# Kernel optimization log

Hardware: AMD Instinct MI355X
Metric: run time of the kernel (lower is better)

Reference implementation:

```python
import jax, jax.numpy as jnp
import numpy as np

N_NODES = 100000
N_HEDGES = 200000
E = 1200000
N_GRAPHS = 512
H = 64            # h_dim
HE = 35           # hedge_fea_dim (CHGConv default)
HOUT = 128        # hout_dim
L = 3             # n_layers
EPS = 1e-5


def _segment_mean(vals, seg, num):
    s = jax.ops.segment_sum(vals, seg, num_segments=num)
    cnt = jax.ops.segment_sum(jnp.ones((vals.shape[0], 1), vals.dtype), seg, num_segments=num)
    return s / jnp.maximum(cnt, 1.0)


def _bn(v, g, b):
    # BatchNorm1d in training mode: batch mean / biased variance
    m = jnp.mean(v, axis=0)
    var = jnp.var(v, axis=0)
    return g * (v - m) * jax.lax.rsqrt(var + EPS) + b


def _chg_conv(x, node_idx, hedge_idx, hattr,
              Wf1, bf1, Wc1, bc1, Wf2, bf2, Wc2, bc2,
              gf, btf, gc, btc, go, bto):
    # gather node feats into hedges, mean-aggregate per hyperedge
    agg = _segment_mean(x[node_idx], hedge_idx, N_HEDGES)          # [NH, H]
    msg = jnp.concatenate([agg, hattr], axis=1)                    # [NH, H+HE]
    z_f = _bn(msg @ Wf1 + bf1, gf, btf)
    z_c = _bn(msg @ Wc1 + bc1, gc, btc)
    hedge_feats = jax.nn.sigmoid(z_f) * jax.nn.softplus(z_c)       # [NH, HE]
    z = jnp.concatenate([x[node_idx], hedge_feats[hedge_idx]], axis=-1)  # [E, H+HE]
    out = jax.nn.sigmoid(z @ Wf2 + bf2) * jax.nn.softplus(z @ Wc2 + bc2)  # [E, H]
    out = _segment_mean(out, node_idx, N_NODES)                    # [N, H]
    out = _bn(out, go, bto)
    return jax.nn.softplus(out + x)


def setup_inputs() -> dict:
    key = jax.random.key(0)
    ks = jax.random.split(key, 32)
    x = jax.random.normal(ks[0], (N_NODES, 92), dtype=jnp.float32)
    node_idx = jax.random.randint(ks[1], (E,), 0, N_NODES)
    hedge_idx = jax.random.randint(ks[2], (E,), 0, N_HEDGES)
    hyperedge_index = jnp.stack([node_idx, hedge_idx], axis=0)     # [2, E]
    hedge_attr = jax.random.normal(ks[3], (N_HEDGES, HE), dtype=jnp.float32)
    batch = jnp.sort(jax.random.randint(ks[4], (N_NODES,), 0, N_GRAPHS))

    s = 0.05
    d = H + HE
    inp = {
        'x': x, 'hyperedge_index': hyperedge_index, 'hedge_attr': hedge_attr, 'batch': batch,
        'We': jax.random.normal(ks[5], (92, H)) * s, 'be': jnp.zeros((H,)),
        'Wf1': jax.random.normal(ks[6], (L, d, HE)) * s, 'bf1': jnp.zeros((L, HE)),
        'Wc1': jax.random.normal(ks[7], (L, d, HE)) * s, 'bc1': jnp.zeros((L, HE)),
        'Wf2': jax.random.normal(ks[8], (L, d, H)) * s, 'bf2': jnp.zeros((L, H)),
        'Wc2': jax.random.normal(ks[9], (L, d, H)) * s, 'bc2': jnp.zeros((L, H)),
        'bn_f_g': jnp.ones((L, HE)), 'bn_f_b': jnp.zeros((L, HE)),
        'bn_c_g': jnp.ones((L, HE)), 'bn_c_b': jnp.zeros((L, HE)),
        'bn_o_g': jnp.ones((L, H)), 'bn_o_b': jnp.zeros((L, H)),
        'Wl2': jax.random.normal(ks[10], (H, HOUT)) * s, 'bl2': jnp.zeros((HOUT,)),
        'Wo': jax.random.normal(ks[11], (HOUT, 1)) * s, 'bo': jnp.zeros((1,)),
    }
    return inp


def reference(x, hyperedge_index, hedge_attr, batch, We, be,
              Wf1, bf1, Wc1, bc1, Wf2, bf2, Wc2, bc2,
              bn_f_g, bn_f_b, bn_c_g, bn_c_b, bn_o_g, bn_o_b,
              Wl2, bl2, Wo, bo):
    node_idx = hyperedge_index[0]
    hedge_idx = hyperedge_index[1]
    h = x @ We + be                                                # embed 92 -> H
    for i in range(L):                                             # only mconvs are used in forward
        h = _chg_conv(h, node_idx, hedge_idx, hedge_attr,
                      Wf1[i], bf1[i], Wc1[i], bc1[i], Wf2[i], bf2[i], Wc2[i], bc2[i],
                      bn_f_g[i], bn_f_b[i], bn_c_g[i], bn_c_b[i], bn_o_g[i], bn_o_b[i])
        h = jax.nn.relu(h)
    g = _segment_mean(h, batch, N_GRAPHS)                          # [G, H]
    g = jax.nn.softplus(g @ Wl2 + bl2)                             # [G, HOUT]
    return g @ Wo + bo                                             # [G, 1]
```

## Files before the change

### kernel.cpp

```cpp
#include <hip/hip_runtime.h>
#include <cstddef>

#define N_NODES_  100000
#define N_HEDGES_ 200000
#define E_        1200000
#define G_        512
#define H_        64
#define HE_       35
#define D_        99
#define HOUT_     128
#define L_        3
#define NBN5_     196
#define NBH5_     391
#define CHUNK_    4096

typedef unsigned int u32;
typedef _Float16 f2_t __attribute__((ext_vector_type(2)));

__device__ __forceinline__ float sigm_(float x){
  return __builtin_amdgcn_rcpf(1.f + __expf(-x));
}
__device__ __forceinline__ float sp_(float x){
  return fmaxf(x, 0.f) + __logf(1.f + __expf(-fabsf(x)));
}
__device__ __forceinline__ float gate_(float F, float C){ return sigm_(F)*sp_(C); }

__device__ __forceinline__ u32 pk_(float a, float b){
  return __builtin_bit_cast(u32, __builtin_amdgcn_cvt_pkrtz(a, b));
}
__device__ __forceinline__ u32 pkadd_(u32 a, u32 b){
  f2_t s = __builtin_bit_cast(f2_t, a) + __builtin_bit_cast(f2_t, b);
  return __builtin_bit_cast(u32, s);
}
__device__ __forceinline__ float dot2_(u32 a, u32 b, float c){
#if __has_builtin(__builtin_amdgcn_fdot2)
  return __builtin_amdgcn_fdot2(__builtin_bit_cast(f2_t, a),
                                __builtin_bit_cast(f2_t, b), c, false);
#else
  f2_t x = __builtin_bit_cast(f2_t, a), y = __builtin_bit_cast(f2_t, b);
  return c + (float)x[0]*(float)y[0] + (float)x[1]*(float)y[1];
#endif
}
__device__ __forceinline__ float lo_(u32 a){ return (float)__builtin_bit_cast(f2_t, a)[0]; }
__device__ __forceinline__ float hi_(u32 a){ return (float)__builtin_bit_cast(f2_t, a)[1]; }

__global__ void k_gcnt(const int* __restrict__ batch, int* __restrict__ gcnt){
  int n = blockIdx.x*256 + threadIdx.x;
  if (n < N_NODES_) atomicAdd(&gcnt[batch[n]], 1);
}
__global__ void k_gscan(const int* __restrict__ gcnt, int* __restrict__ goff){
  __shared__ int tmp[512];
  int t = threadIdx.x;
  int v = gcnt[t];
  tmp[t] = v; __syncthreads();
  for (int d = 1; d < 512; d <<= 1){
    int x = (t >= d) ? tmp[t-d] : 0; __syncthreads();
    tmp[t] += x; __syncthreads();
  }
  goff[t] = tmp[t] - v;
  if (t == 511) goff[512] = tmp[511];
}

__global__ void k_bhist(const int* __restrict__ ni, const int* __restrict__ hi,
                        int* __restrict__ totN, int* __restrict__ totH){
  __shared__ int hN[NBN5_], hH[NBH5_];
  for (int i = threadIdx.x; i < NBN5_; i += 256) hN[i] = 0;
  for (int i = threadIdx.x; i < NBH5_; i += 256) hH[i] = 0;
  __syncthreads();
  int stride = gridDim.x*256;
  for (int e = blockIdx.x*256 + threadIdx.x; e < E_; e += stride){
    atomicAdd(&hN[ni[e] >> 9], 1);
    atomicAdd(&hH[hi[e] >> 9], 1);
  }
  __syncthreads();
  for (int i = threadIdx.x; i < NBN5_; i += 256) if (hN[i]) atomicAdd(&totN[i], hN[i]);
  for (int i = threadIdx.x; i < NBH5_; i += 256) if (hH[i]) atomicAdd(&totH[i], hH[i]);
}

__global__ void k_bscan(const int* __restrict__ totN, const int* __restrict__ totH,
                        int* __restrict__ bbaseN, int* __restrict__ bbaseH,
                        int* __restrict__ gcurN, int* __restrict__ gcurH){
  __shared__ int tmp[512];
  int t = threadIdx.x;
  int v = (t < NBN5_) ? totN[t] : 0;
  tmp[t] = v; __syncthreads();
  for (int d = 1; d < 512; d <<= 1){
    int x = (t >= d) ? tmp[t-d] : 0; __syncthreads();
    tmp[t] += x; __syncthreads();
  }
  if (t < NBN5_){ int b = tmp[t] - v; bbaseN[t] = b; gcurN[t] = b; }
  __syncthreads();
  int w = (t < NBH5_) ? totH[t] : 0;
  tmp[t] = w; __syncthreads();
  for (int d = 1; d < 512; d <<= 1){
    int x = (t >= d) ? tmp[t-d] : 0; __syncthreads();
    tmp[t] += x; __syncthreads();
  }
  if (t < NBH5_){ int b = tmp[t] - w; bbaseH[t] = b; gcurH[t] = b; }
}

__global__ void k_binfill(const int* __restrict__ ni, const int* __restrict__ hi,
                          int* __restrict__ gcurN, int* __restrict__ gcurH,
                          u32* __restrict__ pairN, u32* __restrict__ pairH){
  __shared__ int histN[NBN5_], histH[NBH5_];
  __shared__ int baseN[NBN5_], baseH[NBH5_];
  const int nchunks = (E_ + CHUNK_ - 1)/CHUNK_;
  for (int c = blockIdx.x; c < nchunks; c += gridDim.x){
    int e0 = c*CHUNK_;
    int e1 = e0 + CHUNK_; if (e1 > E_) e1 = E_;
    for (int i = threadIdx.x; i < NBN5_; i += 256) histN[i] = 0;
    for (int i = threadIdx.x; i < NBH5_; i += 256) histH[i] = 0;
    __syncthreads();
    for (int e = e0 + threadIdx.x; e < e1; e += 256){
      atomicAdd(&histN[ni[e] >> 9], 1);
      atomicAdd(&histH[hi[e] >> 9], 1);
    }
    __syncthreads();
    for (int i = threadIdx.x; i < NBN5_; i += 256){
      int hv = histN[i];
      baseN[i] = hv ? atomicAdd(&gcurN[i], hv) : 0;
      histN[i] = 0;
    }
    for (int i = threadIdx.x; i < NBH5_; i += 256){
      int hv = histH[i];
      baseH[i] = hv ? atomicAdd(&gcurH[i], hv) : 0;
      histH[i] = 0;
    }
    __syncthreads();
    for (int e = e0 + threadIdx.x; e < e1; e += 256){
      int n = ni[e], he = hi[e];
      int bn = n >> 9, bh = he >> 9;
      int pn = baseN[bn] + atomicAdd(&histN[bn], 1);
      pairN[pn] = ((u32)(n & 511) << 18) | (u32)he;
      int ph = baseH[bh] + atomicAdd(&histH[bh], 1);
      pairH[ph] = ((u32)(he & 511) << 18) | (u32)n;
    }
    __syncthreads();
  }
}

__global__ void __launch_bounds__(512) k_csrfill2(
    const int* __restrict__ bbase, const int* __restrict__ gcur,
    const u32* __restrict__ pair, int nrows, int* __restrict__ out,
    int* __restrict__ off_arr, int* __restrict__ cnt_arr, float* __restrict__ inv_arr){
  __shared__ int cnt[512], cur[512], tmp[512];
  int b = blockIdx.x, t = threadIdx.x;
  int nb = b*512;
  cnt[t] = 0;
  __syncthreads();
  int base = bbase[b], end = gcur[b];
  for (int pos = base + t; pos < end; pos += 512)
    atomicAdd(&cnt[pair[pos] >> 18], 1);
  __syncthreads();
  int v = cnt[t];
  tmp[t] = v; __syncthreads();
  for (int d = 1; d < 512; d <<= 1){
    int x = (t >= d) ? tmp[t-d] : 0; __syncthreads();
    tmp[t] += x; __syncthreads();
  }
  int ro = base + tmp[t] - v;
  cur[t] = ro;
  int row = nb + t;
  if (row < nrows){
    off_arr[row] = ro;
    cnt_arr[row] = v;
    inv_arr[row] = 1.f/fmaxf((float)v, 1.f);
  }
  __syncthreads();
  for (int pos = base + t; pos < end; pos += 512){
    u32 p = pair[pos];
    int idx = atomicAdd(&cur[p >> 18], 1);
    out[idx] = (int)(p & 0x3FFFFu);
  }
}

__global__ void k_hattr_pack(const float* __restrict__ hattr, u32* __restrict__ hattr16){
  int i = blockIdx.x*256 + threadIdx.x;
  if (i >= N_HEDGES_*18) return;
  int he = i/18, p = i - he*18;
  int k0 = 2*p, k1 = 2*p + 1;
  float w0 = (k0 < 35) ? hattr[(size_t)he*35 + k0] : 0.f;
  float w1 = (k1 < 35) ? hattr[(size_t)he*35 + k1] : 0.f;
  hattr16[i] = pk_(w0, w1);
}

__global__ void k_embed(const float* __restrict__ x, const float* __restrict__ We,
                        const float* __restrict__ be, u32* __restrict__ h16){
  __shared__ __align__(16) float As[64*100];
  __shared__ __align__(16) float Ws[64*100];
  int tid = threadIdx.x;
  for (int idx = tid; idx < 64*100; idx += 256){
    int c = idx/100, k = idx - c*100;
    Ws[idx] = (k < 92) ? We[k*64 + c] : 0.f;
  }
  int rt = tid & 15, ct = tid >> 4;
  float bias[4];
  #pragma unroll
  for (int j = 0; j < 4; ++j) bias[j] = be[ct*4 + j];
  const int ntiles = (N_NODES_ + 63)/64;
  for (int tile = blockIdx.x; tile < ntiles; tile += gridDim.x){
    int rbase = tile*64;
    __syncthreads();
    for (int idx = tid; idx < 64*100; idx += 256){
      int r = idx/100, k = idx - r*100;
      int rg = rbase + r;
      As[idx] = (rg < N_NODES_ && k < 92) ? x[(size_t)rg*92 + k] : 0.f;
    }
    __syncthreads();
    float acc[4][4] = {};
    for (int kc = 0; kc < 25; ++kc){
      float4 av[4], wv[4];
      #pragma unroll
      for (int i = 0; i < 4; ++i) av[i] = *(const float4*)&As[(rt + 16*i)*100 + kc*4];
      #pragma unroll
      for (int j = 0; j < 4; ++j) wv[j] = *(const float4*)&Ws[(ct*4 + j)*100 + kc*4];
      #pragma unroll
      for (int i = 0; i < 4; ++i)
        #pragma unroll
        for (int j = 0; j < 4; ++j)
          acc[i][j] += av[i].x*wv[j].x + av[i].y*wv[j].y + av[i].z*wv[j].z + av[i].w*wv[j].w;
    }
    #pragma unroll
    for (int i = 0; i < 4; ++i){
      int r = rbase + rt + 16*i;
      if (r < N_NODES_){
        h16[(size_t)r*32 + ct*2]     = pk_(acc[i][0] + bias[0], acc[i][1] + bias[1]);
        h16[(size_t)r*32 + ct*2 + 1] = pk_(acc[i][2] + bias[2], acc[i][3] + bias[3]);
      }
    }
  }
}

__global__ void __launch_bounds__(256) k_gather_hedge(
    const u32* __restrict__ h16, const int* __restrict__ hedge_off,
    const int* __restrict__ hcnt, const int* __restrict__ edge_h,
    const float* __restrict__ hinv, u32* __restrict__ hmean16){
  int w = (blockIdx.x*256 + threadIdx.x) >> 3;
  int p = threadIdx.x & 7;
  if (w >= N_HEDGES_) return;
  int off = hedge_off[w], deg = hcnt[w];
  float a[8] = {};
  int i = 0;
  for (; i + 1 < deg; i += 2){
    int n0 = edge_h[off+i], n1 = edge_h[off+i+1];
    uint4 u0 = *(const uint4*)&h16[(size_t)n0*32 + 4*p];
    uint4 u1 = *(const uint4*)&h16[(size_t)n1*32 + 4*p];
    a[0] += lo_(u0.x) + lo_(u1.x); a[1] += hi_(u0.x) + hi_(u1.x);
    a[2] += lo_(u0.y) + lo_(u1.y); a[3] += hi_(u0.y) + hi_(u1.y);
    a[4] += lo_(u0.z) + lo_(u1.z); a[5] += hi_(u0.z) + hi_(u1.z);
    a[6] += lo_(u0.w) + lo_(u1.w); a[7] += hi_(u0.w) + hi_(u1.w);
  }
  if (i < deg){
    uint4 u = *(const uint4*)&h16[(size_t)edge_h[off+i]*32 + 4*p];
    a[0] += lo_(u.x); a[1] += hi_(u.x); a[2] += lo_(u.y); a[3] += hi_(u.y);
    a[4] += lo_(u.z); a[5] += hi_(u.z); a[6] += lo_(u.w); a[7] += hi_(u.w);
  }
  float inv = hinv[w];
  uint4 st;
  st.x = pk_(a[0]*inv, a[1]*inv); st.y = pk_(a[2]*inv, a[3]*inv);
  st.z = pk_(a[4]*inv, a[5]*inv); st.w = pk_(a[6]*inv, a[7]*inv);
  *(uint4*)&hmean16[(size_t)w*32 + 4*p] = st;
}

__global__ void k_hedge_mlp1(const u32* __restrict__ hmean16, const u32* __restrict__ hattr16,
                             const float* __restrict__ Wf1, const float* __restrict__ bf1,
                             const float* __restrict__ Wc1, const float* __restrict__ bc1,
                             __fp16* __restrict__ tfc16T, float* __restrict__ hstats){
  __shared__ __align__(16) u32 As16[64*52];
  __shared__ __align__(16) u32 Ws16[80*52];
  __shared__ float sstat[160];
  int tid = threadIdx.x;
  for (int idx = tid; idx < 80*52; idx += 256){
    int c = idx/52, kk = idx - c*52;
    int k0 = 2*kk, k1 = 2*kk + 1;
    float w0 = 0.f, w1 = 0.f;
    if (c < 70){
      if (k0 < 99) w0 = (c < 35) ? Wf1[k0*35 + c] : Wc1[k0*35 + (c-35)];
      if (k1 < 99) w1 = (c < 35) ? Wf1[k1*35 + c] : Wc1[k1*35 + (c-35)];
    }
    Ws16[idx] = pk_(w0, w1);
  }
  for (int idx = tid; idx < 160; idx += 256) sstat[idx] = 0.f;
  int rt = tid & 15, ct = tid >> 4;
  float bias[5];
  #pragma unroll
  for (int j = 0; j < 5; ++j){
    int c = ct*5 + j;
    bias[j] = (c < 35) ? bf1[c] : (c < 70 ? bc1[c - 35] : 0.f);
  }
  float sreg[5] = {}, qreg[5] = {};
  for (int tile = blockIdx.x; tile < N_HEDGES_/64; tile += gridDim.x){
    int rbase = tile*64;
    __syncthreads();
    for (int idx = tid; idx < 64*52; idx += 256){
      int r = idx/52, kk = idx - r*52;
      int rg = rbase + r;
      u32 v = 0;
      if (kk < 32)      v = hmean16[(size_t)rg*32 + kk];
      else if (kk < 50) v = hattr16[(size_t)rg*18 + (kk - 32)];
      As16[idx] = v;
    }
    __syncthreads();
    float acc[4][5] = {};
    for (int kc = 0; kc < 13; ++kc){
      uint4 av[4], wv[5];
      #pragma unroll
      for (int i = 0; i < 4; ++i) av[i] = *(const uint4*)&As16[(rt + 16*i)*52 + kc*4];
      #pragma unroll
      for (int j = 0; j < 5; ++j) wv[j] = *(const uint4*)&Ws16[(ct*5 + j)*52 + kc*4];
      #pragma unroll
      for (int i = 0; i < 4; ++i)
        #pragma unroll
        for (int j = 0; j < 5; ++j){
          float a = acc[i][j];
          a = dot2_(av[i].x, wv[j].x, a);
          a = dot2_(av[i].y, wv[j].y, a);
          a = dot2_(av[i].z, wv[j].z, a);
          a = dot2_(av[i].w, wv[j].w, a);
          acc[i][j] = a;
        }
    }
    #pragma unroll
    for (int j = 0; j < 5; ++j){
      int c = ct*5 + j;
      if (c < 70){
        #pragma unroll
        for (int i = 0; i < 4; ++i){
          float v = acc[i][j] + bias[j];
          tfc16T[(size_t)c*N_HEDGES_ + rbase + rt + 16*i] = (__fp16)v;
          sreg[j] += v; qreg[j] += v*v;
        }
      }
    }
  }
  int lane = tid & 63;
  #pragma unroll
  for (int j = 0; j < 5; ++j){
    float s = sreg[j], q = qreg[j];
    #pragma unroll
    for (int m = 1; m < 16; m <<= 1){
      s += __shfl_xor(s, m);
      q += __shfl_xor(q, m);
    }
    if ((lane & 15) == 0){
      int c = ct*5 + j;
      if (c < 70){
        atomicAdd(&sstat[c], s);
        atomicAdd(&sstat[80 + c], q);
      }
    }
  }
  __syncthreads();
  for (int idx = tid; idx < 160; idx += 256) atomicAdd(&hstats[idx], sstat[idx]);
}

__global__ void k_bn_fin_hedge(const float* __restrict__ stats,
                               const float* __restrict__ gf, const float* __restrict__ btf,
                               const float* __restrict__ gc, const float* __restrict__ btc,
                               float* __restrict__ ab, float invN){
  int j = threadIdx.x;
  if (j >= 70) return;
  float m = stats[j]*invN;
  float var = stats[80+j]*invN - m*m;
  float gg = (j < 35) ? gf[j] : gc[j-35];
  float bb = (j < 35) ? btf[j] : btc[j-35];
  float a = gg*rsqrtf(var + 1e-5f);
  ab[j] = a; ab[70+j] = bb - m*a;
}

__global__ void k_hedge_feats(const __fp16* __restrict__ tfc16T, const float* __restrict__ ab,
                              const float* __restrict__ Wf2, const float* __restrict__ bf2,
                              const float* __restrict__ Wc2, const float* __restrict__ bc2,
                              u32* __restrict__ heFC2){
  __shared__ __align__(16) u32 As16[64*20];
  __shared__ __align__(16) u32 Ws16[128*20];
  int tid = threadIdx.x;
  for (int idx = tid; idx < 128*20; idx += 256){
    int c = idx/20, kk = idx - c*20;
    int k0 = 2*kk, k1 = 2*kk + 1;
    float w0 = 0.f, w1 = 0.f;
    if (k0 < 35) w0 = (c < 64) ? Wf2[(64+k0)*64 + c] : Wc2[(64+k0)*64 + (c-64)];
    if (k1 < 35) w1 = (c < 64) ? Wf2[(64+k1)*64 + c] : Wc2[(64+k1)*64 + (c-64)];
    Ws16[idx] = pk_(w0, w1);
  }
  int rt = tid & 15, ct = tid >> 4;
  float biasF[4], biasC[4];
  #pragma unroll
  for (int j = 0; j < 4; ++j){ biasF[j] = bf2[ct*4 + j]; biasC[j] = bc2[ct*4 + j]; }
  for (int tile = blockIdx.x; tile < N_HEDGES_/64; tile += gridDim.x){
    int rbase = tile*64;
    __syncthreads();
    for (int idx = tid; idx < 64*20; idx += 256){
      int kk = idx >> 6;
      int r  = idx & 63;
      float a0 = 0.f, a1 = 0.f;
      if (kk < 18){
        int rg = rbase + r;
        int k0 = 2*kk, k1 = 2*kk + 1;
        {
          float tf = (float)tfc16T[(size_t)k0*N_HEDGES_ + rg];
          float tc = (float)tfc16T[(size_t)(35+k0)*N_HEDGES_ + rg];
          float zf = ab[k0]*tf + ab[70 + k0];
          float zc = ab[35+k0]*tc + ab[105 + k0];
          a0 = gate_(zf, zc);
        }
        if (k1 < 35){
          float tf = (float)tfc16T[(size_t)k1*N_HEDGES_ + rg];
          float tc = (float)tfc16T[(size_t)(35+k1)*N_HEDGES_ + rg];
          float zf = ab[k1]*tf + ab[70 + k1];
          float zc = ab[35+k1]*tc + ab[105 + k1];
          a1 = gate_(zf, zc);
        }
      }
      As16[r*20 + kk] = pk_(a0, a1);
    }
    __syncthreads();
    float accF[4][4] = {}, accC[4][4] = {};
    for (int kc = 0; kc < 5; ++kc){
      uint4 av[4], wF[4], wC[4];
      #pragma unroll
      for (int i = 0; i < 4; ++i) av[i] = *(const uint4*)&As16[(rt + 16*i)*20 + kc*4];
      #pragma unroll
      for (int j = 0; j < 4; ++j){
        wF[j] = *(const uint4*)&Ws16[(ct*4 + j)*20 + kc*4];
        wC[j] = *(const uint4*)&Ws16[(64 + ct*4 + j)*20 + kc*4];
      }
      #pragma unroll
      for (int i = 0; i < 4; ++i)
        #pragma unroll
        for (int j = 0; j < 4; ++j){
          float f = accF[i][j], c = accC[i][j];
          f = dot2_(av[i].x, wF[j].x, f); c = dot2_(av[i].x, wC[j].x, c);
          f = dot2_(av[i].y, wF[j].y, f); c = dot2_(av[i].y, wC[j].y, c);
          f = dot2_(av[i].z, wF[j].z, f); c = dot2_(av[i].z, wC[j].z, c);
          f = dot2_(av[i].w, wF[j].w, f); c = dot2_(av[i].w, wC[j].w, c);
          accF[i][j] = f; accC[i][j] = c;
        }
    }
    #pragma unroll
    for (int i = 0; i < 4; ++i){
      int r = rbase + rt + 16*i;
      #pragma unroll
      for (int j = 0; j < 4; ++j){
        heFC2[(size_t)r*64 + ct*4 + j] = pk_(accF[i][j] + biasF[j], accC[i][j] + biasC[j]);
      }
    }
  }
}

__global__ void k_node_lin(const u32* __restrict__ h16,
                           const float* __restrict__ Wf2, const float* __restrict__ Wc2,
                           u32* __restrict__ nFC2){
  __shared__ __align__(16) u32 As16[64*36];
  __shared__ __align__(16) u32 Ws16[128*36];
  int tid = threadIdx.x;
  for (int idx = tid; idx < 128*36; idx += 256){
    int c = idx/36, kk = idx - c*36;
    int k0 = 2*kk, k1 = 2*kk + 1;
    float w0 = 0.f, w1 = 0.f;
    if (k0 < 64) w0 = (c < 64) ? Wf2[k0*64 + c] : Wc2[k0*64 + (c-64)];
    if (k1 < 64) w1 = (c < 64) ? Wf2[k1*64 + c] : Wc2[k1*64 + (c-64)];
    Ws16[idx] = pk_(w0, w1);
  }
  int rt = tid & 15, ct = tid >> 4;
  const int ntiles = (N_NODES_ + 63)/64;
  for (int tile = blockIdx.x; tile < ntiles; tile += gridDim.x){
    int rbase = tile*64;
    __syncthreads();
    for (int idx = tid; idx < 64*36; idx += 256){
      int r = idx/36, kk = idx - r*36;
      int rg = rbase + r;
      As16[idx] = (rg < N_NODES_ && kk < 32) ? h16[(size_t)rg*32 + kk] : 0u;
    }
    __syncthreads();
    float accF[4][4] = {}, accC[4][4] = {};
    for (int kc = 0; kc < 8; ++kc){
      uint4 av[4], wF[4], wC[4];
      #pragma unroll
      for (int i = 0; i < 4; ++i) av[i] = *(const uint4*)&As16[(rt + 16*i)*36 + kc*4];
      #pragma unroll
      for (int j = 0; j < 4; ++j){
        wF[j] = *(const uint4*)&Ws16[(ct*4 + j)*36 + kc*4];
        wC[j] = *(const uint4*)&Ws16[(64 + ct*4 + j)*36 + kc*4];
      }
      #pragma unroll
      for (int i = 0; i < 4; ++i)
        #pragma unroll
        for (int j = 0; j < 4; ++j){
          float f = accF[i][j], c = accC[i][j];
          f = dot2_(av[i].x, wF[j].x, f); c = dot2_(av[i].x, wC[j].x, c);
          f = dot2_(av[i].y, wF[j].y, f); c = dot2_(av[i].y, wC[j].y, c);
          f = dot2_(av[i].z, wF[j].z, f); c = dot2_(av[i].z, wC[j].z, c);
          f = dot2_(av[i].w, wF[j].w, f); c = dot2_(av[i].w, wC[j].w, c);
          accF[i][j] = f; accC[i][j] = c;
        }
    }
    #pragma unroll
    for (int i = 0; i < 4; ++i){
      int r = rbase + rt + 16*i;
      if (r < N_NODES_){
        #pragma unroll
        for (int j = 0; j < 4; ++j){
          nFC2[(size_t)r*64 + ct*4 + j] = pk_(accF[i][j], accC[i][j]);
        }
      }
    }
  }
}

__global__ void k_edge(const u32* __restrict__ nFC2, const u32* __restrict__ heFC2,
                       const int* __restrict__ node_off, const int* __restrict__ ndeg,
                       const int* __restrict__ edge_n, const float* __restrict__ ninv,
                       __fp16* __restrict__ nmean16, float* __restrict__ nstats){
  int lane = threadIdx.x & 63, wave = threadIdx.x >> 6;
  float s = 0.f, q = 0.f;
  for (int base = blockIdx.x*4; base < N_NODES_; base += gridDim.x*4){
    int n = base + wave;
    if (n < N_NODES_){
      int off = __builtin_amdgcn_readfirstlane(node_off[n]);
      int deg = __builtin_amdgcn_readfirstlane(ndeg[n]);
      u32 p0 = nFC2[(size_t)n*64 + lane];
      float acc = 0.f;
      int i = 0;
      for (; i + 7 < deg; i += 8){
        int e0 = edge_n[off+i],   e1 = edge_n[off+i+1], e2 = edge_n[off+i+2], e3 = edge_n[off+i+3];
        int e4 = edge_n[off+i+4], e5 = edge_n[off+i+5], e6 = edge_n[off+i+6], e7 = edge_n[off+i+7];
        u32 s0 = pkadd_(p0, heFC2[(size_t)e0*64 + lane]);
        u32 s1 = pkadd_(p0, heFC2[(size_t)e1*64 + lane]);
        u32 s2 = pkadd_(p0, heFC2[(size_t)e2*64 + lane]);
        u32 s3 = pkadd_(p0, heFC2[(size_t)e3*64 + lane]);
        u32 s4 = pkadd_(p0, heFC2[(size_t)e4*64 + lane]);
        u32 s5 = pkadd_(p0, heFC2[(size_t)e5*64 + lane]);
        u32 s6 = pkadd_(p0, heFC2[(size_t)e6*64 + lane]);
        u32 s7 = pkadd_(p0, heFC2[(size_t)e7*64 + lane]);
        acc += gate_(lo_(s0), hi_(s0)) + gate_(lo_(s1), hi_(s1))
             + gate_(lo_(s2), hi_(s2)) + gate_(lo_(s3), hi_(s3))
             + gate_(lo_(s4), hi_(s4)) + gate_(lo_(s5), hi_(s5))
             + gate_(lo_(s6), hi_(s6)) + gate_(lo_(s7), hi_(s7));
      }
      for (; i + 3 < deg; i += 4){
        int e0 = edge_n[off+i], e1 = edge_n[off+i+1], e2 = edge_n[off+i+2], e3 = edge_n[off+i+3];
        u32 s0 = pkadd_(p0, heFC2[(size_t)e0*64 + lane]);
        u32 s1 = pkadd_(p0, heFC2[(size_t)e1*64 + lane]);
        u32 s2 = pkadd_(p0, heFC2[(size_t)e2*64 + lane]);
        u32 s3 = pkadd_(p0, heFC2[(size_t)e3*64 + lane]);
        acc += gate_(lo_(s0), hi_(s0)) + gate_(lo_(s1), hi_(s1))
             + gate_(lo_(s2), hi_(s2)) + gate_(lo_(s3), hi_(s3));
      }
      for (; i < deg; ++i){
        u32 sA = pkadd_(p0, heFC2[(size_t)edge_n[off+i]*64 + lane]);
        acc += gate_(lo_(sA), hi_(sA));
      }
      float m = acc * ninv[n];
      nmean16[(size_t)n*64 + lane] = (__fp16)m;
      s += m; q += m*m;
    }
  }
  __shared__ float p1[256], p2[256];
  p1[threadIdx.x] = s; p2[threadIdx.x] = q;
  __syncthreads();
  if (wave == 0){
    float a = p1[lane] + p1[64+lane] + p1[128+lane] + p1[192+lane];
    float b = p2[lane] + p2[64+lane] + p2[128+lane] + p2[192+lane];
    atomicAdd(&nstats[lane], a);
    atomicAdd(&nstats[64+lane], b);
  }
}

__global__ void k_bn_fin_node(const float* __restrict__ stats, const float* __restrict__ g,
                              const float* __restrict__ bt, float* __restrict__ ab, float invN){
  int j = threadIdx.x;
  if (j >= 64) return;
  float m = stats[j]*invN;
  float var = stats[64+j]*invN - m*m;
  float a = g[j]*rsqrtf(var + 1e-5f);
  ab[j] = a; ab[64+j] = bt[j] - m*a;
}

__global__ void k_node_update(const u32* __restrict__ nmean16, const float* __restrict__ ab,
                              const u32* __restrict__ h16, u32* __restrict__ h16out){
  int t = blockIdx.x*256 + threadIdx.x;
  if (t >= N_NODES_*32) return;
  int p = t & 31;
  int f0 = 2*p, f1 = 2*p + 1;
  u32 nm = nmean16[t];
  u32 hh = h16[t];
  float r0 = sp_(ab[f0]*lo_(nm) + ab[64+f0] + lo_(hh));
  float r1 = sp_(ab[f1]*hi_(nm) + ab[64+f1] + hi_(hh));
  h16out[t] = pk_(r0, r1);
}

__global__ void __launch_bounds__(256) k_graph_agg2(
    const u32* __restrict__ h16, const int* __restrict__ goff,
    float* __restrict__ gmean){
  __shared__ float s0[256], s1[256];
  int g = blockIdx.x;
  int st = goff[g], en = goff[g+1];
  int p = threadIdx.x & 31;
  int r = threadIdx.x >> 5;
  float a0 = 0.f, a1 = 0.f;
  for (int n = st + r; n < en; n += 8){
    u32 u = h16[(size_t)n*32 + p];
    a0 += lo_(u); a1 += hi_(u);
  }
  s0[threadIdx.x] = a0; s1[threadIdx.x] = a1;
  __syncthreads();
  for (int d = 128; d >= 32; d >>= 1){
    if (threadIdx.x < d){
      s0[threadIdx.x] += s0[threadIdx.x + d];
      s1[threadIdx.x] += s1[threadIdx.x + d];
    }
    __syncthreads();
  }
  if (threadIdx.x < 32){
    float inv = 1.f/fmaxf((float)(en - st), 1.f);
    gmean[(size_t)g*64 + 2*threadIdx.x]     = s0[threadIdx.x]*inv;
    gmean[(size_t)g*64 + 2*threadIdx.x + 1] = s1[threadIdx.x]*inv;
  }
}

__global__ void k_head(const float* __restrict__ gmean,
                       const float* __restrict__ Wl2, const float* __restrict__ bl2,
                       const float* __restrict__ Wo, const float* __restrict__ bo,
                       float* __restrict__ out){
  __shared__ float gm[64];
  __shared__ float red[128];
  int g = blockIdx.x, j = threadIdx.x;
  if (j < 64) gm[j] = gmean[(size_t)g*64+j];
  __syncthreads();
  float u = bl2[j];
  for (int f = 0; f < 64; ++f) u += gm[f]*Wl2[f*128+j];
  red[j] = sp_(u)*Wo[j];
  __syncthreads();
  for (int s = 64; s > 0; s >>= 1){
    if (j < s) red[j] += red[j+s];
    __syncthreads();
  }
  if (j == 0) out[g] = red[0] + bo[0];
}

extern "C" void kernel_launch(void* const* d_in, const int* in_sizes, int n_in,
                              void* d_out, int out_size, void* d_ws, size_t ws_size,
                              hipStream_t stream){
  (void)in_sizes; (void)n_in; (void)out_size; (void)ws_size;
  const float* x      = (const float*)d_in[0];
  const int*   ni     = (const int*)d_in[1];
  const int*   hi     = ni + E_;
  const float* hattr  = (const float*)d_in[2];
  const int*   batch  = (const int*)d_in[3];
  const float* We     = (const float*)d_in[4];
  const float* be     = (const float*)d_in[5];
  const float* Wf1    = (const float*)d_in[6];
  const float* bf1    = (const float*)d_in[7];
  const float* Wc1    = (const float*)d_in[8];
  const float* bc1    = (const float*)d_in[9];
  const float* Wf2    = (const float*)d_in[10];
  const float* bf2    = (const float*)d_in[11];
  const float* Wc2    = (const float*)d_in[12];
  const float* bc2    = (const float*)d_in[13];
  const float* bn_f_g = (const float*)d_in[14];
  const float* bn_f_b = (const float*)d_in[15];
  const float* bn_c_g = (const float*)d_in[16];
  const float* bn_c_b = (const float*)d_in[17];
  const float* bn_o_g = (const float*)d_in[18];
  const float* bn_o_b = (const float*)d_in[19];
  const float* Wl2    = (const float*)d_in[20];
  const float* bl2    = (const float*)d_in[21];
  const float* Wo     = (const float*)d_in[22];
  const float* bo     = (const float*)d_in[23];

  float* ws = (float*)d_ws;
  size_t o = 0;
  __fp16* tfc16T = (__fp16*)(ws + o); o += (size_t)N_HEDGES_*70/2 + 64;
  u32*   nFC2  = (u32*)tfc16T;
  u32*   pairN = (u32*)tfc16T;
  u32*   pairH = pairN + E_;
  float* hmR   = ws + o; o += (size_t)N_HEDGES_*H_;
  u32*   hmean16 = (u32*)hmR;
  u32*   heFC2   = (u32*)hmR;
  __fp16* nmean16 = (__fp16*)(ws + o); o += (size_t)N_NODES_*H_/2 + 64;
  u32*  h16a   = (u32*)(ws + o); o += (size_t)N_NODES_*32;
  u32*  h16b   = (u32*)(ws + o); o += (size_t)N_NODES_*32;
  u32*  hattr16= (u32*)(ws + o); o += (size_t)N_HEDGES_*18;
  float* hstats = ws + o; o += 256;
  float* habs   = ws + o; o += 256;
  float* nstats = ws + o; o += 128;
  float* nabs   = ws + o; o += 128;
  float* gmean  = ws + o; o += (size_t)G_*H_;
  float* hinv   = ws + o; o += N_HEDGES_;
  float* ninv   = ws + o; o += N_NODES_;
  int* hcnt     = (int*)(ws + o); o += N_HEDGES_;
  int* ndeg     = (int*)(ws + o); o += N_NODES_;
  int* gcnt     = (int*)(ws + o); o += G_;
  int* goff     = (int*)(ws + o); o += G_ + 1;
  int* node_off = (int*)(ws + o); o += N_NODES_;
  int* hedge_off= (int*)(ws + o); o += N_HEDGES_;
  int* gcurN    = (int*)(ws + o); o += NBN5_;
  int* gcurH    = (int*)(ws + o); o += NBH5_;
  int* totN     = (int*)(ws + o); o += NBN5_;
  int* totH     = (int*)(ws + o); o += NBH5_;
  int* bbaseN   = (int*)(ws + o); o += NBN5_;
  int* bbaseH   = (int*)(ws + o); o += NBH5_;
  int* edge_n   = (int*)(ws + o); o += E_;
  int* edge_h   = (int*)(ws + o); o += E_;

  hipMemsetAsync(totN, 0, sizeof(int)*(NBN5_ + NBH5_), stream);
  hipMemsetAsync(gcnt, 0, sizeof(int)*G_, stream);

  k_gcnt<<<(N_NODES_+255)/256, 256, 0, stream>>>(batch, gcnt);
  k_gscan<<<1, 512, 0, stream>>>(gcnt, goff);
  k_hattr_pack<<<(N_HEDGES_*18+255)/256, 256, 0, stream>>>(hattr, hattr16);

  k_bhist<<<512, 256, 0, stream>>>(ni, hi, totN, totH);
  k_bscan<<<1, 512, 0, stream>>>(totN, totH, bbaseN, bbaseH, gcurN, gcurH);
  k_binfill<<<(E_+CHUNK_-1)/CHUNK_, 256, 0, stream>>>(ni, hi, gcurN, gcurH, pairN, pairH);
  k_csrfill2<<<NBN5_, 512, 0, stream>>>(bbaseN, gcurN, pairN, N_NODES_, edge_n,
                                        node_off, ndeg, ninv);
  k_csrfill2<<<NBH5_, 512, 0, stream>>>(bbaseH, gcurH, pairH, N_HEDGES_, edge_h,
                                        hedge_off, hcnt, hinv);

  k_embed<<<768, 256, 0, stream>>>(x, We, be, h16a);

  u32* hc16 = h16a;
  u32* hn16 = h16b;
  for (int l = 0; l < L_; ++l){
    const float* Wf1l = Wf1 + (size_t)l*D_*HE_;
    const float* Wc1l = Wc1 + (size_t)l*D_*HE_;
    const float* Wf2l = Wf2 + (size_t)l*D_*H_;
    const float* Wc2l = Wc2 + (size_t)l*D_*H_;

    hipMemsetAsync(hstats, 0, sizeof(float)*160, stream);
    hipMemsetAsync(nstats, 0, sizeof(float)*128, stream);

    k_gather_hedge<<<(N_HEDGES_*8+255)/256, 256, 0, stream>>>(hc16, hedge_off, hcnt, edge_h,
                                                              hinv, hmean16);
    k_hedge_mlp1<<<1280, 256, 0, stream>>>(hmean16, hattr16, Wf1l, bf1 + l*HE_,
                                           Wc1l, bc1 + l*HE_, tfc16T, hstats);
    k_bn_fin_hedge<<<1, 128, 0, stream>>>(hstats, bn_f_g + l*HE_, bn_f_b + l*HE_,
                                          bn_c_g + l*HE_, bn_c_b + l*HE_, habs,
                                          1.f/(float)N_HEDGES_);
    k_hedge_feats<<<1536, 256, 0, stream>>>(tfc16T, habs, Wf2l, bf2 + l*H_,
                                            Wc2l, bc2 + l*H_, heFC2);
    k_node_lin<<<1024, 256, 0, stream>>>(hc16, Wf2l, Wc2l, nFC2);
    k_edge<<<2048, 256, 0, stream>>>(nFC2, heFC2, node_off, ndeg, edge_n, ninv,
                                     nmean16, nstats);
    k_bn_fin_node<<<1, 64, 0, stream>>>(nstats, bn_o_g + l*H_, bn_o_b + l*H_, nabs,
                                        1.f/(float)N_NODES_);
    k_node_update<<<(N_NODES_*32+255)/256, 256, 0, stream>>>((const u32*)nmean16, nabs,
                                                             hc16, hn16);
    u32* t3 = hc16; hc16 = hn16; hn16 = t3;
  }

  k_graph_agg2<<<G_, 256, 0, stream>>>(hc16, goff, gmean);
  k_head<<<G_, 128, 0, stream>>>(gmean, Wl2, bl2, Wo, bo, (float*)d_out);
}
```

Before: 1.184 ms.

## Use MFMA f16 matrix ops for hedge MLP1 and stage transposed output via LDS

Replaces the per-thread dot2 register-tiled GEMM in the hyperedge MLP kernel with 16x16x32 f16 MFMA instructions. Each wave handles 16 rows across 5 column tiles, and the LDS row stride is padded to cover K=128. Results are written transposed into LDS and then stored to the transposed fp16 output with 16-byte vector writes, which should cut ALU work and scattered 2-byte global stores. This adds an extra LDS round trip and barriers per tile, and the padding does some wasted MFMA work on zeroed K entries.

```diff
diff --git a/kernel.cpp b/kernel.cpp
--- a/kernel.cpp
+++ b/kernel.cpp
@@ -16,6 +16,8 @@
 
 typedef unsigned int u32;
 typedef _Float16 f2_t __attribute__((ext_vector_type(2)));
+typedef _Float16 h8_t __attribute__((ext_vector_type(8)));
+typedef float f32x4 __attribute__((ext_vector_type(4)));
 
 __device__ __forceinline__ float sigm_(float x){
   return __builtin_amdgcn_rcpf(1.f + __expf(-x));
@@ -266,34 +268,37 @@
                              const float* __restrict__ Wf1, const float* __restrict__ bf1,
                              const float* __restrict__ Wc1, const float* __restrict__ bc1,
                              __fp16* __restrict__ tfc16T, float* __restrict__ hstats){
-  __shared__ __align__(16) u32 As16[64*52];
-  __shared__ __align__(16) u32 Ws16[80*52];
+  __shared__ __align__(16) u32 As16[64*68];
+  __shared__ __align__(16) u32 Ws16[80*68];
   __shared__ float sstat[160];
   int tid = threadIdx.x;
-  for (int idx = tid; idx < 80*52; idx += 256){
-    int c = idx/52, kk = idx - c*52;
-    int k0 = 2*kk, k1 = 2*kk + 1;
+  for (int idx = tid; idx < 80*68; idx += 256){
+    int c = idx/68, kk = idx - c*68;
+    int k0 = 2*kk, k1 = k0 + 1;
     float w0 = 0.f, w1 = 0.f;
     if (c < 70){
-      if (k0 < 99) w0 = (c < 35) ? Wf1[k0*35 + c] : Wc1[k0*35 + (c-35)];
-      if (k1 < 99) w1 = (c < 35) ? Wf1[k1*35 + c] : Wc1[k1*35 + (c-35)];
+      int cc = (c < 35) ? c : c - 35;
+      const float* W = (c < 35) ? Wf1 : Wc1;
+      if (k0 < 99) w0 = W[k0*35 + cc];
+      if (k1 < 99) w1 = W[k1*35 + cc];
     }
     Ws16[idx] = pk_(w0, w1);
   }
   for (int idx = tid; idx < 160; idx += 256) sstat[idx] = 0.f;
-  int rt = tid & 15, ct = tid >> 4;
+  int lane = tid & 63, wv = tid >> 6;
+  int l15 = lane & 15, lg = lane >> 4;
   float bias[5];
   #pragma unroll
-  for (int j = 0; j < 5; ++j){
-    int c = ct*5 + j;
-    bias[j] = (c < 35) ? bf1[c] : (c < 70 ? bc1[c - 35] : 0.f);
+  for (int t = 0; t < 5; ++t){
+    int c = t*16 + l15;
+    bias[t] = (c < 35) ? bf1[c] : (c < 70 ? bc1[c - 35] : 0.f);
   }
   float sreg[5] = {}, qreg[5] = {};
   for (int tile = blockIdx.x; tile < N_HEDGES_/64; tile += gridDim.x){
     int rbase = tile*64;
     __syncthreads();
-    for (int idx = tid; idx < 64*52; idx += 256){
-      int r = idx/52, kk = idx - r*52;
+    for (int idx = tid; idx < 64*68; idx += 256){
+      int r = idx/68, kk = idx - r*68;
       int rg = rbase + r;
       u32 v = 0;
       if (kk < 32)      v = hmean16[(size_t)rg*32 + kk];
@@ -301,49 +306,50 @@
       As16[idx] = v;
     }
     __syncthreads();
-    float acc[4][5] = {};
-    for (int kc = 0; kc < 13; ++kc){
-      uint4 av[4], wv[5];
-      #pragma unroll
-      for (int i = 0; i < 4; ++i) av[i] = *(const uint4*)&As16[(rt + 16*i)*52 + kc*4];
-      #pragma unroll
-      for (int j = 0; j < 5; ++j) wv[j] = *(const uint4*)&Ws16[(ct*5 + j)*52 + kc*4];
-      #pragma unroll
-      for (int i = 0; i < 4; ++i)
-        #pragma unroll
-        for (int j = 0; j < 5; ++j){
-          float a = acc[i][j];
-          a = dot2_(av[i].x, wv[j].x, a);
-          a = dot2_(av[i].y, wv[j].y, a);
-          a = dot2_(av[i].z, wv[j].z, a);
-          a = dot2_(av[i].w, wv[j].w, a);
-          acc[i][j] = a;
-        }
-    }
+    h8_t af[4];
+    int arow = wv*16 + l15;
     #pragma unroll
-    for (int j = 0; j < 5; ++j){
-      int c = ct*5 + j;
-      if (c < 70){
-        #pragma unroll
-        for (int i = 0; i < 4; ++i){
-          float v = acc[i][j] + bias[j];
-          tfc16T[(size_t)c*N_HEDGES_ + rbase + rt + 16*i] = (__fp16)v;
-          sreg[j] += v; qreg[j] += v*v;
-        }
-      }
-    }
-  }
-  int lane = tid & 63;
+    for (int ks = 0; ks < 4; ++ks)
+      af[ks] = *(const h8_t*)&As16[arow*68 + ks*16 + lg*4];
+    __syncthreads();
+    __fp16* Cs = (__fp16*)As16;
+    f32x4 acc[5];
+    #pragma unroll
+    for (int t = 0; t < 5; ++t) acc[t] = (f32x4){0.f,0.f,0.f,0.f};
+    #pragma unroll
+    for (int t = 0; t < 5; ++t){
+      int bcol = t*16 + l15;
+      #pragma unroll
+      for (int ks = 0; ks < 4; ++ks){
+        h8_t bf = *(const h8_t*)&Ws16[bcol*68 + ks*16 + lg*4];
+        acc[t] = __builtin_amdgcn_mfma_f32_16x16x32_f16(af[ks], bf, acc[t], 0, 0, 0);
+      }
+    }
+    #pragma unroll
+    for (int t = 0; t < 5; ++t){
+      int col = t*16 + l15;
+      #pragma unroll
+      for (int q = 0; q < 4; ++q){
+        float v = acc[t][q] + bias[t];
+        int row = wv*16 + lg*4 + q;
+        Cs[col*72 + row] = (__fp16)v;
+        sreg[t] += v; qreg[t] += v*v;
+      }
+    }
+    __syncthreads();
+    for (int idx = tid; idx < 70*8; idx += 256){
+      int col = idx >> 3, seg = idx & 7;
+      uint4 v = *(const uint4*)&Cs[col*72 + seg*8];
+      *(uint4*)&tfc16T[(size_t)col*N_HEDGES_ + rbase + seg*8] = v;
+    }
+  }
   #pragma unroll
-  for (int j = 0; j < 5; ++j){
-    float s = sreg[j], q = qreg[j];
-    #pragma unroll
-    for (int m = 1; m < 16; m <<= 1){
-      s += __shfl_xor(s, m);
-      q += __shfl_xor(q, m);
-    }
-    if ((lane & 15) == 0){
-      int c = ct*5 + j;
+  for (int t = 0; t < 5; ++t){
+    float s = sreg[t], q = qreg[t];
+    s += __shfl_xor(s, 16); q += __shfl_xor(q, 16);
+    s += __shfl_xor(s, 32); q += __shfl_xor(q, 32);
+    if (lg == 0){
+      int c = t*16 + l15;
       if (c < 70){
         atomicAdd(&sstat[c], s);
         atomicAdd(&sstat[80 + c], q);
```

New measurement: 1.161 ms. About the same (-1.9%).
